# Performance work log

Measured on AMD Instinct MI355X. Metric: run time of the kernel, lower is better.

The kernel has to match this reference:

```python
import jax, jax.numpy as jnp
import numpy as np

B, C, H, W, HEADS = 2, 128, 56, 56, 4
ASYM_W = 0.5


def setup_inputs() -> dict:
    key = jax.random.key(0)
    ks = jax.random.split(key, 9)
    s = lambda k, shape: jax.random.normal(k, shape, jnp.float32) * 0.02
    inner = C  # dim_head * heads == dim
    return {
        "x": jax.random.normal(ks[0], (B, C, H, W), jnp.float32),
        "Wq": s(ks[1], (inner, C)),
        "Wk": s(ks[2], (inner, C)),
        "Wv": s(ks[3], (inner, C)),
        "Wo": s(ks[4], (C, inner)),
        "bo": jnp.zeros((C,), jnp.float32),
        "Wa1": s(ks[5], (C, 2 * C)),
        "ba1": jnp.zeros((C,), jnp.float32),
        "Wa2": s(ks[6], (1, C)),
        "ba2": jnp.zeros((1,), jnp.float32),
    }


def _conv1x1(Wmat, t, bias=None):
    # 1x1 conv == per-pixel matmul over channels
    out = jnp.einsum('oc,bchw->bohw', Wmat, t)
    if bias is not None:
        out = out + bias[None, :, None, None]
    return out


def reference(x, Wq, Wk, Wv, Wo, bo, Wa1, ba1, Wa2, ba2):
    b, c, h, w = x.shape
    heads = HEADS
    dh = c // heads
    scale = dh ** -0.5

    # ---- asymmetry map ----
    left = x[:, :, :, : w // 2]
    right = x[:, :, :, w // 2:]
    right_flipped = right[:, :, :, ::-1]
    mw = min(left.shape[3], right_flipped.shape[3])
    cat = jnp.concatenate([left[:, :, :, :mw], right_flipped[:, :, :, :mw]], axis=1)
    a = _conv1x1(Wa1, cat, ba1)
    a = jax.nn.gelu(a, approximate=False)  # torch default GELU is exact erf
    a = _conv1x1(Wa2, a, ba2)
    a = jax.nn.sigmoid(a)
    # bilinear, align_corners=False == half-pixel convention of jax.image.resize
    asym = jax.image.resize(a, (b, 1, h, w), method='linear')

    # ---- q/k/v projections ----
    def heads_split(t):  # b (h d) x y -> b h (x y) d
        return t.reshape(b, heads, dh, h * w).transpose(0, 1, 3, 2)

    q = heads_split(_conv1x1(Wq, x))
    k = heads_split(_conv1x1(Wk, x))
    v = heads_split(_conv1x1(Wv, x))

    dots = jnp.einsum('bhid,bhjd->bhij', q, k) * scale  # [b,h,hw,hw]

    # 3x3 neighborhood mask, vectorized
    idx = jnp.arange(h * w)
    ii, jj = idx // w, idx % w
    mask = ((jnp.abs(ii[:, None] - ii[None, :]) <= 1)
            & (jnp.abs(jj[:, None] - jj[None, :]) <= 1)).astype(dots.dtype)
    dots = dots * mask + (1.0 - mask) * -1e9

    attn = jax.nn.softmax(dots, axis=-1)
    out = jnp.einsum('bhij,bhjd->bhid', attn, v)
    out = out.transpose(0, 1, 3, 2).reshape(b, c, h, w)  # b h (x y) d -> b (h d) x y

    out = out * (1.0 + ASYM_W * asym)
    return _conv1x1(Wo, out, bo)
```

## Files before the change

kernel.cpp:

```cpp
#include <hip/hip_runtime.h>
#include <hip/hip_bf16.h>
#include <math.h>

#define B_ 2
#define C_ 128
#define H_ 56
#define W_ 56
#define N_ (H_*W_)
#define HEADS_ 4
#define DH_ 32
#define MW_ 28
#define NPOS_ (H_*MW_)

typedef unsigned short ushort_t;
typedef __bf16 v8bf __attribute__((ext_vector_type(8)));
typedef float  v4f  __attribute__((ext_vector_type(4)));

#define MFMA16(a,b,c) __builtin_amdgcn_mfma_f32_16x16x32_bf16((a),(b),(c),0,0,0)

__device__ __forceinline__ unsigned short f2bf(float f) {
    return __builtin_bit_cast(unsigned short, __float2bfloat16(f));
}
__device__ __forceinline__ unsigned int bfpack(float a, float b) {
    return (unsigned int)f2bf(a) | ((unsigned int)f2bf(b) << 16);
}
__device__ __forceinline__ void unpack8(uint4 u, float* f) {
    f[0] = __uint_as_float(u.x << 16); f[1] = __uint_as_float(u.x & 0xffff0000u);
    f[2] = __uint_as_float(u.y << 16); f[3] = __uint_as_float(u.y & 0xffff0000u);
    f[4] = __uint_as_float(u.z << 16); f[5] = __uint_as_float(u.z & 0xffff0000u);
    f[6] = __uint_as_float(u.w << 16); f[7] = __uint_as_float(u.w & 0xffff0000u);
}

__global__ __launch_bounds__(256)
void qkv_asym_kernel(const float* __restrict__ x,
                     const float* __restrict__ Wq, const float* __restrict__ Wk,
                     const float* __restrict__ Wv,
                     const float* __restrict__ Wa1, const float* __restrict__ ba1,
                     const float* __restrict__ Wa2, const float* __restrict__ ba2,
                     ushort_t* __restrict__ q, ushort_t* __restrict__ k,
                     ushort_t* __restrict__ v, float* __restrict__ aval) {
    __shared__ __align__(16) char smem[35840];
    const int t = threadIdx.x;
    const int b = blockIdx.z;
    const int wv_ = t >> 6;
    const int l   = t & 63;
    const int lr  = l & 15;
    const int lq  = l >> 4;

    if (blockIdx.y < 6) {
        ushort_t* WT = (ushort_t*)smem;
        ushort_t* XT = (ushort_t*)(smem + 17408);

        const int n0   = blockIdx.x * 64;
        const int mIdx = blockIdx.y >> 1;
        const int o0   = (blockIdx.y & 1) * 64;
        const float* W  = (mIdx == 0 ? Wq : (mIdx == 1 ? Wk : Wv));
        ushort_t* dst   = (mIdx == 0 ? q  : (mIdx == 1 ? k  : v ));
        const float* xb = x + (size_t)b * C_ * N_;

        for (int it = 0; it < 8; ++it) {
            int idx = t + it * 256;
            int row = idx >> 5, f4 = idx & 31;
            float4 w4 = *(const float4*)(W + (size_t)(o0 + row) * C_ + f4 * 4);
            ushort4 p4 = { f2bf(w4.x), f2bf(w4.y), f2bf(w4.z), f2bf(w4.w) };
            *(ushort4*)(WT + row * 136 + f4 * 4) = p4;
        }
        {
            int px = t & 63, g = t >> 6;
            const float* xc = xb + n0 + px;
            for (int it = 0; it < 8; ++it) {
                int c0 = (g + it * 4) * 4;
                float a0 = xc[(size_t)(c0 + 0) * N_];
                float a1 = xc[(size_t)(c0 + 1) * N_];
                float a2 = xc[(size_t)(c0 + 2) * N_];
                float a3 = xc[(size_t)(c0 + 3) * N_];
                ushort4 p4 = { f2bf(a0), f2bf(a1), f2bf(a2), f2bf(a3) };
                *(ushort4*)(XT + px * 136 + c0) = p4;
            }
        }
        __syncthreads();

        v4f acc[4];
        #pragma unroll
        for (int nt = 0; nt < 4; ++nt) acc[nt] = (v4f){0.f, 0.f, 0.f, 0.f};

        #pragma unroll
        for (int ks = 0; ks < 4; ++ks) {
            v8bf af = *(const v8bf*)(WT + (wv_ * 16 + lr) * 136 + ks * 32 + lq * 8);
            #pragma unroll
            for (int nt = 0; nt < 4; ++nt) {
                v8bf bfr = *(const v8bf*)(XT + (nt * 16 + lr) * 136 + ks * 32 + lq * 8);
                acc[nt] = MFMA16(af, bfr, acc[nt]);
            }
        }

        __syncthreads();
        ushort_t* epT = WT;
        #pragma unroll
        for (int nt = 0; nt < 4; ++nt) {
            uint2 pk;
            pk.x = bfpack(acc[nt][0], acc[nt][1]);
            pk.y = bfpack(acc[nt][2], acc[nt][3]);
            *(uint2*)(epT + (nt * 16 + lr) * 136 + wv_ * 16 + lq * 4) = pk;
        }
        __syncthreads();
        for (int it = 0; it < 2; ++it) {
            int idx = t + it * 256;
            int px = idx >> 3, g = idx & 7;
            *(uint4*)(dst + ((size_t)b * N_ + n0 + px) * C_ + o0 + g * 8) =
                *(const uint4*)(epT + px * 136 + g * 8);
        }
    } else {
        ushort_t* wa  = (ushort_t*)smem;
        ushort_t* cat = (ushort_t*)(smem + 18432);
        float* wred   = (float*)(smem + 35328);

        const int P0 = blockIdx.x * 32;
        const float* xb = x + (size_t)b * C_ * N_;

        {
            int pos = t & 31, chg = t >> 5;
            int pg = P0 + pos;
            int h = pg / MW_, j = pg - h * MW_;
            int col = (chg < 4) ? (h * W_ + j) : (h * W_ + (W_ - 1 - j));
            int cbase = (chg & 3) * 32;
            const float* src = xb + col;
            ushort_t* crow = cat + pos * 264 + chg * 32;
            #pragma unroll
            for (int u = 0; u < 16; ++u) {
                float f0 = src[(size_t)(cbase + 2 * u) * N_];
                float f1 = src[(size_t)(cbase + 2 * u + 1) * N_];
                ushort2 pp = { f2bf(f0), f2bf(f1) };
                *(ushort2*)(crow + 2 * u) = pp;
            }
        }

        v4f acc2[2][2];
        #pragma unroll
        for (int mi = 0; mi < 2; ++mi)
            #pragma unroll
            for (int nt = 0; nt < 2; ++nt) acc2[mi][nt] = (v4f){0.f, 0.f, 0.f, 0.f};

        for (int kc = 0; kc < 4; ++kc) {
            __syncthreads();
            for (int it = 0; it < 8; ++it) {
                int idx = t + it * 256;
                int row = idx >> 4, f4 = idx & 15;
                float4 w4 = *(const float4*)(Wa1 + (size_t)row * 256 + kc * 64 + f4 * 4);
                ushort4 p4 = { f2bf(w4.x), f2bf(w4.y), f2bf(w4.z), f2bf(w4.w) };
                *(ushort4*)(wa + row * 72 + f4 * 4) = p4;
            }
            __syncthreads();
            #pragma unroll
            for (int ks = 0; ks < 2; ++ks) {
                v8bf a0f = *(const v8bf*)(wa + ((2*wv_ + 0) * 16 + lr) * 72 + ks * 32 + lq * 8);
                v8bf a1f = *(const v8bf*)(wa + ((2*wv_ + 1) * 16 + lr) * 72 + ks * 32 + lq * 8);
                v8bf b0f = *(const v8bf*)(cat + lr * 264        + kc * 64 + ks * 32 + lq * 8);
                v8bf b1f = *(const v8bf*)(cat + (16 + lr) * 264 + kc * 64 + ks * 32 + lq * 8);
                acc2[0][0] = MFMA16(a0f, b0f, acc2[0][0]);
                acc2[0][1] = MFMA16(a0f, b1f, acc2[0][1]);
                acc2[1][0] = MFMA16(a1f, b0f, acc2[1][0]);
                acc2[1][1] = MFMA16(a1f, b1f, acc2[1][1]);
            }
        }

        float p2[2] = {0.f, 0.f};
        #pragma unroll
        for (int mi = 0; mi < 2; ++mi) {
            #pragma unroll
            for (int r = 0; r < 4; ++r) {
                int m = (2*wv_ + mi) * 16 + lq * 4 + r;
                float wa2v = Wa2[m];
                float b1v  = ba1[m];
                #pragma unroll
                for (int nt = 0; nt < 2; ++nt) {
                    float val = acc2[mi][nt][r] + b1v;
                    float gl = 0.5f * val * (1.0f + erff(val * 0.7071067811865475f));
                    p2[nt] += gl * wa2v;
                }
            }
        }
        #pragma unroll
        for (int nt = 0; nt < 2; ++nt) {
            p2[nt] += __shfl_xor(p2[nt], 16, 64);
            p2[nt] += __shfl_xor(p2[nt], 32, 64);
        }
        if (l < 16) {
            wred[wv_ * 32 + lr]      = p2[0];
            wred[wv_ * 32 + 16 + lr] = p2[1];
        }
        __syncthreads();
        if (t < 32) {
            float s = wred[t] + wred[32 + t] + wred[64 + t] + wred[96 + t] + ba2[0];
            aval[(size_t)b * NPOS_ + P0 + t] = 1.0f / (1.0f + expf(-s));
        }
    }
}

__global__ __launch_bounds__(256)
void attn_oproj_kernel(const ushort_t* __restrict__ q, const ushort_t* __restrict__ k,
                       const ushort_t* __restrict__ v, const float* __restrict__ aval,
                       const float* __restrict__ Wo, const float* __restrict__ bo,
                       float* __restrict__ out) {
    __shared__ __align__(16) char smem[45056];
    ushort_t* WoT = (ushort_t*)smem;
    ushort_t* aoT = (ushort_t*)(smem + 34816);
    float*    ep  = (float*)(smem + 34816);

    const int t  = threadIdx.x;
    const int n0 = blockIdx.x * 16;
    const int b  = blockIdx.y;

    for (int it = 0; it < 16; ++it) {
        int idx = t + it * 256;
        int row = idx >> 5, f4 = idx & 31;
        float4 w4 = *(const float4*)(Wo + (size_t)row * C_ + f4 * 4);
        ushort4 p4 = { f2bf(w4.x), f2bf(w4.y), f2bf(w4.z), f2bf(w4.w) };
        *(ushort4*)(WoT + row * 136 + f4 * 4) = p4;
    }

    const size_t base = (size_t)b * N_ * C_;
    {
        int s = t & 3, head = (t >> 2) & 3, p = t >> 4;
        int n = n0 + p;
        int i = n / W_, j = n - i * W_;
        int dbase = head * DH_ + s * 8;

        float qf[8];
        unpack8(*(const uint4*)(q + base + (size_t)n * C_ + dbase), qf);

        float dts[9]; int mm[9];
        #pragma unroll
        for (int tt = 0; tt < 9; ++tt) {
            int di = tt / 3 - 1, dj = tt % 3 - 1;
            int ii = i + di, jj = j + dj;
            bool ok = ((unsigned)ii < (unsigned)H_) && ((unsigned)jj < (unsigned)W_);
            int m = ok ? ii * W_ + jj : n;
            mm[tt] = m;
            float kf[8];
            unpack8(*(const uint4*)(k + base + (size_t)m * C_ + dbase), kf);
            float pd = qf[0]*kf[0] + qf[1]*kf[1] + qf[2]*kf[2] + qf[3]*kf[3]
                     + qf[4]*kf[4] + qf[5]*kf[5] + qf[6]*kf[6] + qf[7]*kf[7];
            pd += __shfl_xor(pd, 1, 64);
            pd += __shfl_xor(pd, 2, 64);
            dts[tt] = ok ? pd * 0.17677669529663687f : -1e30f;
        }
        float mx = dts[0];
        #pragma unroll
        for (int tt = 1; tt < 9; ++tt) mx = fmaxf(mx, dts[tt]);
        float sum = 0.f;
        #pragma unroll
        for (int tt = 0; tt < 9; ++tt) { dts[tt] = expf(dts[tt] - mx); sum += dts[tt]; }
        const float inv = 1.0f / sum;

        float acc[8] = {0,0,0,0,0,0,0,0};
        #pragma unroll
        for (int tt = 0; tt < 9; ++tt) {
            float vf[8];
            unpack8(*(const uint4*)(v + base + (size_t)mm[tt] * C_ + dbase), vf);
            float wt = dts[tt] * inv;
            #pragma unroll
            for (int d = 0; d < 8; ++d) acc[d] += wt * vf[d];
        }

        float f = 0.5f * (float)j - 0.25f;
        f = fminf(fmaxf(f, 0.0f), 27.0f);
        int i0 = (int)f; if (i0 > 26) i0 = 26;
        float frac = f - (float)i0;
        const float* av = aval + (size_t)b * NPOS_ + i * MW_;
        float a = av[i0] * (1.0f - frac) + av[i0 + 1] * frac;
        float sc = 1.0f + 0.5f * a;

        uint4 o;
        o.x = bfpack(acc[0] * sc, acc[1] * sc);
        o.y = bfpack(acc[2] * sc, acc[3] * sc);
        o.z = bfpack(acc[4] * sc, acc[5] * sc);
        o.w = bfpack(acc[6] * sc, acc[7] * sc);
        *(uint4*)(aoT + p * 136 + dbase) = o;
    }
    __syncthreads();

    const int wv_ = t >> 6, l = t & 63, lr = l & 15, lq = l >> 4;
    v4f acc4[2];
    acc4[0] = (v4f){0.f, 0.f, 0.f, 0.f};
    acc4[1] = (v4f){0.f, 0.f, 0.f, 0.f};

    #pragma unroll
    for (int ks = 0; ks < 4; ++ks) {
        v8bf b0 = *(const v8bf*)(aoT + lr * 136 + ks * 32 + lq * 8);
        #pragma unroll
        for (int mi = 0; mi < 2; ++mi) {
            v8bf af = *(const v8bf*)(WoT + ((wv_ * 2 + mi) * 16 + lr) * 136 + ks * 32 + lq * 8);
            acc4[mi] = MFMA16(af, b0, acc4[mi]);
        }
    }
    __syncthreads();

    #pragma unroll
    for (int mi = 0; mi < 2; ++mi) {
        int o = (wv_ * 2 + mi) * 16 + lq * 4;
        float4 bv = *(const float4*)(bo + o);
        const float bvr[4] = { bv.x, bv.y, bv.z, bv.w };
        #pragma unroll
        for (int r = 0; r < 4; ++r)
            ep[(o + r) * 20 + lr] = acc4[mi][r] + bvr[r];
    }
    __syncthreads();
    for (int it = 0; it < 2; ++it) {
        int idx = t + it * 256;
        int o = idx >> 2, f4 = idx & 3;
        *(float4*)(out + (size_t)b * C_ * N_ + (size_t)o * N_ + n0 + f4 * 4) =
            *(const float4*)(ep + o * 20 + f4 * 4);
    }
}

extern "C" void kernel_launch(void* const* d_in, const int* in_sizes, int n_in,
                              void* d_out, int out_size, void* d_ws, size_t ws_size,
                              hipStream_t stream) {
    const float* x   = (const float*)d_in[0];
    const float* Wq  = (const float*)d_in[1];
    const float* Wk  = (const float*)d_in[2];
    const float* Wv  = (const float*)d_in[3];
    const float* Wo  = (const float*)d_in[4];
    const float* bo  = (const float*)d_in[5];
    const float* Wa1 = (const float*)d_in[6];
    const float* ba1 = (const float*)d_in[7];
    const float* Wa2 = (const float*)d_in[8];
    const float* ba2 = (const float*)d_in[9];
    float* out = (float*)d_out;

    const size_t PXC = (size_t)B_ * N_ * C_;
    ushort_t* qb  = (ushort_t*)d_ws;
    ushort_t* kb  = qb + PXC;
    ushort_t* vb  = kb + PXC;
    float*    aval = (float*)(vb + PXC);

    qkv_asym_kernel<<<dim3(49, 7, B_), 256, 0, stream>>>(
        x, Wq, Wk, Wv, Wa1, ba1, Wa2, ba2, qb, kb, vb, aval);
    attn_oproj_kernel<<<dim3(196, B_), 256, 0, stream>>>(qb, kb, vb, aval, Wo, bo, out);
}
```

Measured before the change: 88.11 us.

## Fuse QKV, asymmetry map, attention and output projection into one kernel

Replaces the two-kernel pipeline (QKV+asym writing bf16 q/k/v to global workspace, then attention+oproj) with a single kernel per (row, half-row, batch). Each block loads a 3x30 halo of x into LDS, computes K/V for the halo and Q for its own 28 pixels, plus the asymmetry row, then does attention and the output projection entirely in LDS. This removes the global round-trip of q/k/v and the second launch. In exchange it recomputes K/V for halo pixels (about 3.2x redundant K/V work) and restages all four weight matrices in every block, with a 130KB LDS footprint and only 224 blocks of 512 threads.

Measured after the change: 87.13 us. Within noise of the previous version (-1.1%).

```diff
diff --git a/kernel.cpp b/kernel.cpp
--- a/kernel.cpp
+++ b/kernel.cpp
@@ -7,10 +7,7 @@
 #define H_ 56
 #define W_ 56
 #define N_ (H_*W_)
-#define HEADS_ 4
-#define DH_ 32
 #define MW_ 28
-#define NPOS_ (H_*MW_)
 
 typedef unsigned short ushort_t;
 typedef __bf16 v8bf __attribute__((ext_vector_type(8)));
@@ -31,214 +28,240 @@
     f[6] = __uint_as_float(u.w << 16); f[7] = __uint_as_float(u.w & 0xffff0000u);
 }
 
-__global__ __launch_bounds__(256)
-void qkv_asym_kernel(const float* __restrict__ x,
-                     const float* __restrict__ Wq, const float* __restrict__ Wk,
-                     const float* __restrict__ Wv,
-                     const float* __restrict__ Wa1, const float* __restrict__ ba1,
-                     const float* __restrict__ Wa2, const float* __restrict__ ba2,
-                     ushort_t* __restrict__ q, ushort_t* __restrict__ k,
-                     ushort_t* __restrict__ v, float* __restrict__ aval) {
-    __shared__ __align__(16) char smem[35840];
-    const int t = threadIdx.x;
-    const int b = blockIdx.z;
-    const int wv_ = t >> 6;
-    const int l   = t & 63;
-    const int lr  = l & 15;
-    const int lq  = l >> 4;
-
-    if (blockIdx.y < 6) {
-        ushort_t* WT = (ushort_t*)smem;
-        ushort_t* XT = (ushort_t*)(smem + 17408);
-
-        const int n0   = blockIdx.x * 64;
-        const int mIdx = blockIdx.y >> 1;
-        const int o0   = (blockIdx.y & 1) * 64;
-        const float* W  = (mIdx == 0 ? Wq : (mIdx == 1 ? Wk : Wv));
-        ushort_t* dst   = (mIdx == 0 ? q  : (mIdx == 1 ? k  : v ));
-        const float* xb = x + (size_t)b * C_ * N_;
-
+#define OFF_W    0
+#define OFF_XT   34816
+#define OFF_KT   60928
+#define OFF_VT   87040
+#define OFF_QT   113152
+#define OFF_AO   121856
+#define OFF_AROW 130560
+#define LDS_TOTAL 130688
+
+#define STAGE_W128(SRC) do {                                                  \
+    _Pragma("unroll")                                                         \
+    for (int it_ = 0; it_ < 8; ++it_) {                                       \
+        int idx_ = t + it_ * 512;                                             \
+        int row_ = idx_ >> 5, f4_ = idx_ & 31;                                \
+        float4 w4_ = *(const float4*)((SRC) + (size_t)row_ * C_ + f4_ * 4);   \
+        ushort4 p4_ = { f2bf(w4_.x), f2bf(w4_.y), f2bf(w4_.z), f2bf(w4_.w) }; \
+        *(ushort4*)(Wb + row_ * 136 + f4_ * 4) = p4_;                         \
+    } } while (0)
+
+__global__ __launch_bounds__(512, 2)
+void fused_kernel(const float* __restrict__ x,
+                  const float* __restrict__ Wq, const float* __restrict__ Wk,
+                  const float* __restrict__ Wv, const float* __restrict__ Wo,
+                  const float* __restrict__ bo,
+                  const float* __restrict__ Wa1, const float* __restrict__ ba1,
+                  const float* __restrict__ Wa2, const float* __restrict__ ba2,
+                  float* __restrict__ out) {
+    extern __shared__ __align__(16) char smem[];
+    ushort_t* Wb   = (ushort_t*)(smem + OFF_W);
+    ushort_t* XT   = (ushort_t*)(smem + OFF_XT);
+    ushort_t* kT   = (ushort_t*)(smem + OFF_KT);
+    ushort_t* vT   = (ushort_t*)(smem + OFF_VT);
+    ushort_t* qT   = (ushort_t*)(smem + OFF_QT);
+    ushort_t* ao   = (ushort_t*)(smem + OFF_AO);
+    ushort_t* cat  = (ushort_t*)(smem + OFF_VT);
+    float*    wred = (float*)(smem + OFF_QT);
+    float*    arow = (float*)(smem + OFF_AROW);
+    float*    ep   = (float*)(smem + OFF_XT);
+
+    const int t  = threadIdx.x;
+    const int i  = blockIdx.x;
+    const int j0 = blockIdx.y * MW_;
+    const int b  = blockIdx.z;
+    const float* xb = x + (size_t)b * C_ * N_;
+
+    const int w  = t >> 6;
+    const int l  = t & 63;
+    const int lr = l & 15;
+    const int lq = l >> 4;
+
+    {
+        const int col = t & 31, chg = t >> 5;
+        if (col < 30) {
+            const int cjc = min(max(j0 - 1 + col, 0), W_ - 1);
+            #pragma unroll
+            for (int r = 0; r < 3; ++r) {
+                const int ric = min(max(i - 1 + r, 0), H_ - 1);
+                const float* src = xb + ric * W_ + cjc;
+                float f[8];
+                #pragma unroll
+                for (int u = 0; u < 8; ++u)
+                    f[u] = src[(size_t)(chg * 8 + u) * N_];
+                uint4 o;
+                o.x = bfpack(f[0], f[1]); o.y = bfpack(f[2], f[3]);
+                o.z = bfpack(f[4], f[5]); o.w = bfpack(f[6], f[7]);
+                *(uint4*)(XT + (r * 30 + col) * 136 + chg * 8) = o;
+            }
+        }
+        if (col < MW_) {
+            const int scol = (chg >= 8) ? (W_ - 1 - col) : col;
+            const float* src = xb + (size_t)((chg & 7) * 16) * N_ + i * W_ + scol;
+            float f[16];
+            #pragma unroll
+            for (int u = 0; u < 16; ++u)
+                f[u] = src[(size_t)u * N_];
+            uint4 o0, o1;
+            o0.x = bfpack(f[0], f[1]);  o0.y = bfpack(f[2], f[3]);
+            o0.z = bfpack(f[4], f[5]);  o0.w = bfpack(f[6], f[7]);
+            o1.x = bfpack(f[8], f[9]);  o1.y = bfpack(f[10], f[11]);
+            o1.z = bfpack(f[12], f[13]); o1.w = bfpack(f[14], f[15]);
+            *(uint4*)(cat + col * 264 + chg * 16 + 0) = o0;
+            *(uint4*)(cat + col * 264 + chg * 16 + 8) = o1;
+        }
+    }
+    __syncthreads();
+
+    v4f acc_a[2];
+    acc_a[0] = (v4f){0.f, 0.f, 0.f, 0.f};
+    acc_a[1] = (v4f){0.f, 0.f, 0.f, 0.f};
+    #pragma unroll
+    for (int kc = 0; kc < 2; ++kc) {
+        if (kc) __syncthreads();
+        #pragma unroll
         for (int it = 0; it < 8; ++it) {
-            int idx = t + it * 256;
+            int idx = t + it * 512;
             int row = idx >> 5, f4 = idx & 31;
-            float4 w4 = *(const float4*)(W + (size_t)(o0 + row) * C_ + f4 * 4);
+            float4 w4 = *(const float4*)(Wa1 + (size_t)row * 256 + kc * 128 + f4 * 4);
             ushort4 p4 = { f2bf(w4.x), f2bf(w4.y), f2bf(w4.z), f2bf(w4.w) };
-            *(ushort4*)(WT + row * 136 + f4 * 4) = p4;
-        }
-        {
-            int px = t & 63, g = t >> 6;
-            const float* xc = xb + n0 + px;
-            for (int it = 0; it < 8; ++it) {
-                int c0 = (g + it * 4) * 4;
-                float a0 = xc[(size_t)(c0 + 0) * N_];
-                float a1 = xc[(size_t)(c0 + 1) * N_];
-                float a2 = xc[(size_t)(c0 + 2) * N_];
-                float a3 = xc[(size_t)(c0 + 3) * N_];
-                ushort4 p4 = { f2bf(a0), f2bf(a1), f2bf(a2), f2bf(a3) };
-                *(ushort4*)(XT + px * 136 + c0) = p4;
-            }
+            *(ushort4*)(Wb + row * 136 + f4 * 4) = p4;
         }
         __syncthreads();
-
-        v4f acc[4];
-        #pragma unroll
-        for (int nt = 0; nt < 4; ++nt) acc[nt] = (v4f){0.f, 0.f, 0.f, 0.f};
-
-        #pragma unroll
-        for (int ks = 0; ks < 4; ++ks) {
-            v8bf af = *(const v8bf*)(WT + (wv_ * 16 + lr) * 136 + ks * 32 + lq * 8);
-            #pragma unroll
-            for (int nt = 0; nt < 4; ++nt) {
-                v8bf bfr = *(const v8bf*)(XT + (nt * 16 + lr) * 136 + ks * 32 + lq * 8);
+        #pragma unroll
+        for (int ks = 0; ks < 4; ++ks) {
+            v8bf af = *(const v8bf*)(Wb + (w * 16 + lr) * 136 + ks * 32 + lq * 8);
+            #pragma unroll
+            for (int nt = 0; nt < 2; ++nt) {
+                v8bf bfr = *(const v8bf*)(cat + (nt * 16 + lr) * 264 + kc * 128 + ks * 32 + lq * 8);
+                acc_a[nt] = MFMA16(af, bfr, acc_a[nt]);
+            }
+        }
+    }
+    {
+        float p2[2] = {0.f, 0.f};
+        #pragma unroll
+        for (int r = 0; r < 4; ++r) {
+            int m = w * 16 + lq * 4 + r;
+            float wa2v = Wa2[m], b1v = ba1[m];
+            #pragma unroll
+            for (int nt = 0; nt < 2; ++nt) {
+                float val = acc_a[nt][r] + b1v;
+                float gl = 0.5f * val * (1.0f + erff(val * 0.7071067811865475f));
+                p2[nt] += gl * wa2v;
+            }
+        }
+        #pragma unroll
+        for (int nt = 0; nt < 2; ++nt) {
+            p2[nt] += __shfl_xor(p2[nt], 16, 64);
+            p2[nt] += __shfl_xor(p2[nt], 32, 64);
+        }
+        if (l < 16) {
+            wred[w * 32 + lr]      = p2[0];
+            wred[w * 32 + 16 + lr] = p2[1];
+        }
+    }
+    __syncthreads();
+    if (t < 32) {
+        float s = ba2[0];
+        #pragma unroll
+        for (int ww = 0; ww < 8; ++ww) s += wred[ww * 32 + t];
+        arow[t] = 1.0f / (1.0f + expf(-s));
+    }
+
+    STAGE_W128(Wq);
+    __syncthreads();
+    {
+        v4f acc[2];
+        acc[0] = (v4f){0.f, 0.f, 0.f, 0.f};
+        acc[1] = (v4f){0.f, 0.f, 0.f, 0.f};
+        #pragma unroll
+        for (int ks = 0; ks < 4; ++ks) {
+            v8bf af = *(const v8bf*)(Wb + (w * 16 + lr) * 136 + ks * 32 + lq * 8);
+            #pragma unroll
+            for (int nt = 0; nt < 2; ++nt) {
+                v8bf bfr = *(const v8bf*)(XT + (31 + nt * 16 + lr) * 136 + ks * 32 + lq * 8);
                 acc[nt] = MFMA16(af, bfr, acc[nt]);
             }
         }
-
-        __syncthreads();
-        ushort_t* epT = WT;
-        #pragma unroll
-        for (int nt = 0; nt < 4; ++nt) {
+        #pragma unroll
+        for (int nt = 0; nt < 2; ++nt) {
             uint2 pk;
             pk.x = bfpack(acc[nt][0], acc[nt][1]);
             pk.y = bfpack(acc[nt][2], acc[nt][3]);
-            *(uint2*)(epT + (nt * 16 + lr) * 136 + wv_ * 16 + lq * 4) = pk;
-        }
-        __syncthreads();
-        for (int it = 0; it < 2; ++it) {
-            int idx = t + it * 256;
-            int px = idx >> 3, g = idx & 7;
-            *(uint4*)(dst + ((size_t)b * N_ + n0 + px) * C_ + o0 + g * 8) =
-                *(const uint4*)(epT + px * 136 + g * 8);
-        }
-    } else {
-        ushort_t* wa  = (ushort_t*)smem;
-        ushort_t* cat = (ushort_t*)(smem + 18432);
-        float* wred   = (float*)(smem + 35328);
-
-        const int P0 = blockIdx.x * 32;
-        const float* xb = x + (size_t)b * C_ * N_;
-
-        {
-            int pos = t & 31, chg = t >> 5;
-            int pg = P0 + pos;
-            int h = pg / MW_, j = pg - h * MW_;
-            int col = (chg < 4) ? (h * W_ + j) : (h * W_ + (W_ - 1 - j));
-            int cbase = (chg & 3) * 32;
-            const float* src = xb + col;
-            ushort_t* crow = cat + pos * 264 + chg * 32;
-            #pragma unroll
-            for (int u = 0; u < 16; ++u) {
-                float f0 = src[(size_t)(cbase + 2 * u) * N_];
-                float f1 = src[(size_t)(cbase + 2 * u + 1) * N_];
-                ushort2 pp = { f2bf(f0), f2bf(f1) };
-                *(ushort2*)(crow + 2 * u) = pp;
-            }
-        }
-
-        v4f acc2[2][2];
-        #pragma unroll
-        for (int mi = 0; mi < 2; ++mi)
-            #pragma unroll
-            for (int nt = 0; nt < 2; ++nt) acc2[mi][nt] = (v4f){0.f, 0.f, 0.f, 0.f};
-
-        for (int kc = 0; kc < 4; ++kc) {
-            __syncthreads();
-            for (int it = 0; it < 8; ++it) {
-                int idx = t + it * 256;
-                int row = idx >> 4, f4 = idx & 15;
-                float4 w4 = *(const float4*)(Wa1 + (size_t)row * 256 + kc * 64 + f4 * 4);
-                ushort4 p4 = { f2bf(w4.x), f2bf(w4.y), f2bf(w4.z), f2bf(w4.w) };
-                *(ushort4*)(wa + row * 72 + f4 * 4) = p4;
-            }
-            __syncthreads();
-            #pragma unroll
-            for (int ks = 0; ks < 2; ++ks) {
-                v8bf a0f = *(const v8bf*)(wa + ((2*wv_ + 0) * 16 + lr) * 72 + ks * 32 + lq * 8);
-                v8bf a1f = *(const v8bf*)(wa + ((2*wv_ + 1) * 16 + lr) * 72 + ks * 32 + lq * 8);
-                v8bf b0f = *(const v8bf*)(cat + lr * 264        + kc * 64 + ks * 32 + lq * 8);
-                v8bf b1f = *(const v8bf*)(cat + (16 + lr) * 264 + kc * 64 + ks * 32 + lq * 8);
-                acc2[0][0] = MFMA16(a0f, b0f, acc2[0][0]);
-                acc2[0][1] = MFMA16(a0f, b1f, acc2[0][1]);
-                acc2[1][0] = MFMA16(a1f, b0f, acc2[1][0]);
-                acc2[1][1] = MFMA16(a1f, b1f, acc2[1][1]);
-            }
-        }
-
-        float p2[2] = {0.f, 0.f};
-        #pragma unroll
-        for (int mi = 0; mi < 2; ++mi) {
-            #pragma unroll
-            for (int r = 0; r < 4; ++r) {
-                int m = (2*wv_ + mi) * 16 + lq * 4 + r;
-                float wa2v = Wa2[m];
-                float b1v  = ba1[m];
-                #pragma unroll
-                for (int nt = 0; nt < 2; ++nt) {
-                    float val = acc2[mi][nt][r] + b1v;
-                    float gl = 0.5f * val * (1.0f + erff(val * 0.7071067811865475f));
-                    p2[nt] += gl * wa2v;
-                }
-            }
-        }
-        #pragma unroll
-        for (int nt = 0; nt < 2; ++nt) {
-            p2[nt] += __shfl_xor(p2[nt], 16, 64);
-            p2[nt] += __shfl_xor(p2[nt], 32, 64);
-        }
-        if (l < 16) {
-            wred[wv_ * 32 + lr]      = p2[0];
-            wred[wv_ * 32 + 16 + lr] = p2[1];
-        }
-        __syncthreads();
-        if (t < 32) {
-            float s = wred[t] + wred[32 + t] + wred[64 + t] + wred[96 + t] + ba2[0];
-            aval[(size_t)b * NPOS_ + P0 + t] = 1.0f / (1.0f + expf(-s));
-        }
-    }
-}
-
-__global__ __launch_bounds__(256)
-void attn_oproj_kernel(const ushort_t* __restrict__ q, const ushort_t* __restrict__ k,
-                       const ushort_t* __restrict__ v, const float* __restrict__ aval,
-                       const float* __restrict__ Wo, const float* __restrict__ bo,
-                       float* __restrict__ out) {
-    __shared__ __align__(16) char smem[45056];
-    ushort_t* WoT = (ushort_t*)smem;
-    ushort_t* aoT = (ushort_t*)(smem + 34816);
-    float*    ep  = (float*)(smem + 34816);
-
-    const int t  = threadIdx.x;
-    const int n0 = blockIdx.x * 16;
-    const int b  = blockIdx.y;
-
-    for (int it = 0; it < 16; ++it) {
-        int idx = t + it * 256;
-        int row = idx >> 5, f4 = idx & 31;
-        float4 w4 = *(const float4*)(Wo + (size_t)row * C_ + f4 * 4);
-        ushort4 p4 = { f2bf(w4.x), f2bf(w4.y), f2bf(w4.z), f2bf(w4.w) };
-        *(ushort4*)(WoT + row * 136 + f4 * 4) = p4;
-    }
-
-    const size_t base = (size_t)b * N_ * C_;
-    {
-        int s = t & 3, head = (t >> 2) & 3, p = t >> 4;
-        int n = n0 + p;
-        int i = n / W_, j = n - i * W_;
-        int dbase = head * DH_ + s * 8;
+            *(uint2*)(qT + (nt * 16 + lr) * 136 + w * 16 + lq * 4) = pk;
+        }
+    }
+    __syncthreads();
+    STAGE_W128(Wk);
+    __syncthreads();
+    {
+        v4f acc[6];
+        #pragma unroll
+        for (int nt = 0; nt < 6; ++nt) acc[nt] = (v4f){0.f, 0.f, 0.f, 0.f};
+        #pragma unroll
+        for (int ks = 0; ks < 4; ++ks) {
+            v8bf af = *(const v8bf*)(Wb + (w * 16 + lr) * 136 + ks * 32 + lq * 8);
+            #pragma unroll
+            for (int nt = 0; nt < 6; ++nt) {
+                v8bf bfr = *(const v8bf*)(XT + (nt * 16 + lr) * 136 + ks * 32 + lq * 8);
+                acc[nt] = MFMA16(af, bfr, acc[nt]);
+            }
+        }
+        #pragma unroll
+        for (int nt = 0; nt < 6; ++nt) {
+            uint2 pk;
+            pk.x = bfpack(acc[nt][0], acc[nt][1]);
+            pk.y = bfpack(acc[nt][2], acc[nt][3]);
+            *(uint2*)(kT + (nt * 16 + lr) * 136 + w * 16 + lq * 4) = pk;
+        }
+    }
+    __syncthreads();
+    STAGE_W128(Wv);
+    __syncthreads();
+    {
+        v4f acc[6];
+        #pragma unroll
+        for (int nt = 0; nt < 6; ++nt) acc[nt] = (v4f){0.f, 0.f, 0.f, 0.f};
+        #pragma unroll
+        for (int ks = 0; ks < 4; ++ks) {
+            v8bf af = *(const v8bf*)(Wb + (w * 16 + lr) * 136 + ks * 32 + lq * 8);
+            #pragma unroll
+            for (int nt = 0; nt < 6; ++nt) {
+                v8bf bfr = *(const v8bf*)(XT + (nt * 16 + lr) * 136 + ks * 32 + lq * 8);
+                acc[nt] = MFMA16(af, bfr, acc[nt]);
+            }
+        }
+        #pragma unroll
+        for (int nt = 0; nt < 6; ++nt) {
+            uint2 pk;
+            pk.x = bfpack(acc[nt][0], acc[nt][1]);
+            pk.y = bfpack(acc[nt][2], acc[nt][3]);
+            *(uint2*)(vT + (nt * 16 + lr) * 136 + w * 16 + lq * 4) = pk;
+        }
+    }
+    __syncthreads();
+
+    STAGE_W128(Wo);
+    if (t < 448) {
+        const int jl = t >> 4, head = (t >> 2) & 3, s = t & 3;
+        const int j  = j0 + jl;
+        const int dbase = head * 32 + s * 8;
 
         float qf[8];
-        unpack8(*(const uint4*)(q + base + (size_t)n * C_ + dbase), qf);
-
-        float dts[9]; int mm[9];
+        unpack8(*(const uint4*)(qT + jl * 136 + dbase), qf);
+
+        float dts[9]; int sl9[9];
         #pragma unroll
         for (int tt = 0; tt < 9; ++tt) {
             int di = tt / 3 - 1, dj = tt % 3 - 1;
             int ii = i + di, jj = j + dj;
             bool ok = ((unsigned)ii < (unsigned)H_) && ((unsigned)jj < (unsigned)W_);
-            int m = ok ? ii * W_ + jj : n;
-            mm[tt] = m;
+            int slot = (di + 1) * 30 + (jl + dj + 1);
+            sl9[tt] = slot;
             float kf[8];
-            unpack8(*(const uint4*)(k + base + (size_t)m * C_ + dbase), kf);
+            unpack8(*(const uint4*)(kT + slot * 136 + dbase), kf);
             float pd = qf[0]*kf[0] + qf[1]*kf[1] + qf[2]*kf[2] + qf[3]*kf[3]
                      + qf[4]*kf[4] + qf[5]*kf[5] + qf[6]*kf[6] + qf[7]*kf[7];
             pd += __shfl_xor(pd, 1, 64);
@@ -257,7 +280,7 @@
         #pragma unroll
         for (int tt = 0; tt < 9; ++tt) {
             float vf[8];
-            unpack8(*(const uint4*)(v + base + (size_t)mm[tt] * C_ + dbase), vf);
+            unpack8(*(const uint4*)(vT + sl9[tt] * 136 + dbase), vf);
             float wt = dts[tt] * inv;
             #pragma unroll
             for (int d = 0; d < 8; ++d) acc[d] += wt * vf[d];
@@ -267,8 +290,7 @@
         f = fminf(fmaxf(f, 0.0f), 27.0f);
         int i0 = (int)f; if (i0 > 26) i0 = 26;
         float frac = f - (float)i0;
-        const float* av = aval + (size_t)b * NPOS_ + i * MW_;
-        float a = av[i0] * (1.0f - frac) + av[i0 + 1] * frac;
+        float a = arow[i0] * (1.0f - frac) + arow[i0 + 1] * frac;
         float sc = 1.0f + 0.5f * a;
 
         uint4 o;
@@ -276,47 +298,47 @@
         o.y = bfpack(acc[2] * sc, acc[3] * sc);
         o.z = bfpack(acc[4] * sc, acc[5] * sc);
         o.w = bfpack(acc[6] * sc, acc[7] * sc);
-        *(uint4*)(aoT + p * 136 + dbase) = o;
-    }
-    __syncthreads();
-
-    const int wv_ = t >> 6, l = t & 63, lr = l & 15, lq = l >> 4;
-    v4f acc4[2];
-    acc4[0] = (v4f){0.f, 0.f, 0.f, 0.f};
-    acc4[1] = (v4f){0.f, 0.f, 0.f, 0.f};
-
+        *(uint4*)(ao + jl * 136 + dbase) = o;
+    }
+    __syncthreads();
+
+    {
+        v4f acc[2];
+        acc[0] = (v4f){0.f, 0.f, 0.f, 0.f};
+        acc[1] = (v4f){0.f, 0.f, 0.f, 0.f};
+        #pragma unroll
+        for (int ks = 0; ks < 4; ++ks) {
+            v8bf af = *(const v8bf*)(Wb + (w * 16 + lr) * 136 + ks * 32 + lq * 8);
+            #pragma unroll
+            for (int nt = 0; nt < 2; ++nt) {
+                v8bf bfr = *(const v8bf*)(ao + (nt * 16 + lr) * 136 + ks * 32 + lq * 8);
+                acc[nt] = MFMA16(af, bfr, acc[nt]);
+            }
+        }
+        float4 bv = *(const float4*)(bo + w * 16 + lq * 4);
+        const float bvr[4] = { bv.x, bv.y, bv.z, bv.w };
+        #pragma unroll
+        for (int nt = 0; nt < 2; ++nt)
+            #pragma unroll
+            for (int r = 0; r < 4; ++r)
+                ep[(w * 16 + lq * 4 + r) * 36 + nt * 16 + lr] = acc[nt][r] + bvr[r];
+    }
+    __syncthreads();
     #pragma unroll
-    for (int ks = 0; ks < 4; ++ks) {
-        v8bf b0 = *(const v8bf*)(aoT + lr * 136 + ks * 32 + lq * 8);
-        #pragma unroll
-        for (int mi = 0; mi < 2; ++mi) {
-            v8bf af = *(const v8bf*)(WoT + ((wv_ * 2 + mi) * 16 + lr) * 136 + ks * 32 + lq * 8);
-            acc4[mi] = MFMA16(af, b0, acc4[mi]);
-        }
-    }
-    __syncthreads();
-
-    #pragma unroll
-    for (int mi = 0; mi < 2; ++mi) {
-        int o = (wv_ * 2 + mi) * 16 + lq * 4;
-        float4 bv = *(const float4*)(bo + o);
-        const float bvr[4] = { bv.x, bv.y, bv.z, bv.w };
-        #pragma unroll
-        for (int r = 0; r < 4; ++r)
-            ep[(o + r) * 20 + lr] = acc4[mi][r] + bvr[r];
-    }
-    __syncthreads();
     for (int it = 0; it < 2; ++it) {
-        int idx = t + it * 256;
-        int o = idx >> 2, f4 = idx & 3;
-        *(float4*)(out + (size_t)b * C_ * N_ + (size_t)o * N_ + n0 + f4 * 4) =
-            *(const float4*)(ep + o * 20 + f4 * 4);
+        int idx = t + it * 512;
+        int ch = idx >> 3, q4 = idx & 7;
+        if (q4 < 7) {
+            *(float4*)(out + ((size_t)b * C_ + ch) * N_ + i * W_ + j0 + q4 * 4) =
+                *(const float4*)(ep + ch * 36 + q4 * 4);
+        }
     }
 }
 
 extern "C" void kernel_launch(void* const* d_in, const int* in_sizes, int n_in,
                               void* d_out, int out_size, void* d_ws, size_t ws_size,
                               hipStream_t stream) {
+    (void)in_sizes; (void)n_in; (void)out_size; (void)d_ws; (void)ws_size;
     const float* x   = (const float*)d_in[0];
     const float* Wq  = (const float*)d_in[1];
     const float* Wk  = (const float*)d_in[2];
@@ -329,13 +351,12 @@
     const float* ba2 = (const float*)d_in[9];
     float* out = (float*)d_out;
 
-    const size_t PXC = (size_t)B_ * N_ * C_;
-    ushort_t* qb  = (ushort_t*)d_ws;
-    ushort_t* kb  = qb + PXC;
-    ushort_t* vb  = kb + PXC;
-    float*    aval = (float*)(vb + PXC);
-
-    qkv_asym_kernel<<<dim3(49, 7, B_), 256, 0, stream>>>(
-        x, Wq, Wk, Wv, Wa1, ba1, Wa2, ba2, qb, kb, vb, aval);
-    attn_oproj_kernel<<<dim3(196, B_), 256, 0, stream>>>(qb, kb, vb, aval, Wo, bo, out);
-}
+    static int cfg = 0;
+    if (!cfg) {
+        hipFuncSetAttribute((const void*)fused_kernel,
+                            hipFuncAttributeMaxDynamicSharedMemorySize, LDS_TOTAL);
+        cfg = 1;
+    }
+    fused_kernel<<<dim3(H_, 2, B_), 512, LDS_TOTAL, stream>>>(
+        x, Wq, Wk, Wv, Wo, bo, Wa1, ba1, Wa2, ba2, out);
+}
```
